# Kernel tuning notes

Hardware: AMD Instinct MI355X
Metric: run time of the kernel (lower is better)

The kernel has to match this reference:

```python
import jax, jax.numpy as jnp
import numpy as np

N, H, W, D = 4, 32, 32, 64
NH = 8
L = 4             # num_layers
DFF = 4 * D       # dim_feedforward
PRUNE_RATIO = 0.3
LN_EPS = 1e-5


def setup_inputs() -> dict:
    key = jax.random.key(0)
    ks = jax.random.split(key, 10)
    rn = lambda k, shape: (jax.random.normal(k, shape, dtype=jnp.float32) * 0.02)
    n_keep = int(D * PRUNE_RATIO)
    prune_mask = jnp.concatenate([jnp.ones((n_keep,), jnp.float32), jnp.zeros((D - n_keep,), jnp.float32)])
    return {
        "hsi_features": jax.random.normal(ks[0], (N, H, W, D), dtype=jnp.float32),
        "rgb_features": jax.random.normal(ks[1], (N, H, W, D), dtype=jnp.float32),
        "in_proj_w": rn(ks[2], (L, 3 * D, D)),
        "in_proj_b": jnp.zeros((L, 3 * D), jnp.float32),
        "out_w": rn(ks[3], (L, D, D)),
        "out_b": jnp.zeros((L, D), jnp.float32),
        "lin1_w": rn(ks[4], (L, DFF, D)),
        "lin1_b": jnp.zeros((L, DFF), jnp.float32),
        "lin2_w": rn(ks[5], (L, D, DFF)),
        "lin2_b": jnp.zeros((L, D), jnp.float32),
        "ln1_w": jnp.ones((L, D), jnp.float32),
        "ln1_b": jnp.zeros((L, D), jnp.float32),
        "ln2_w": jnp.ones((L, D), jnp.float32),
        "ln2_b": jnp.zeros((L, D), jnp.float32),
        "prune_mask": prune_mask,
    }


def _ln(x, w, b):
    mu = x.mean(-1, keepdims=True)
    var = ((x - mu) ** 2).mean(-1, keepdims=True)
    return (x - mu) * jax.lax.rsqrt(var + LN_EPS) * w + b


def _encoder_layer(x, p):
    # Post-LN TransformerEncoderLayer (torch default, eval mode -> no dropout).
    in_w, in_b, ow, ob, l1w, l1b, l2w, l2b, n1w, n1b, n2w, n2b = p
    M = x.shape[0]
    hd = D // NH
    qkv = x @ in_w.T + in_b                       # [M, 3D]
    q, k, v = jnp.split(qkv, 3, axis=-1)
    q = q.reshape(M, NH, hd).transpose(1, 0, 2)   # [NH, M, hd]
    k = k.reshape(M, NH, hd).transpose(1, 0, 2)
    v = v.reshape(M, NH, hd).transpose(1, 0, 2)
    scale = 1.0 / jnp.sqrt(jnp.float32(hd))
    att = jax.nn.softmax(jnp.einsum('hmd,hnd->hmn', q * scale, k), axis=-1)  # [NH, M, M]
    o = jnp.einsum('hmn,hnd->hmd', att, v).transpose(1, 0, 2).reshape(M, D)
    o = o @ ow.T + ob
    x = _ln(x + o, n1w, n1b)
    ff = jax.nn.relu(x @ l1w.T + l1b) @ l2w.T + l2b
    return _ln(x + ff, n2w, n2b)


def _mmd(x, y, sigma=1.0):
    # Gaussian-kernel MMD; ||a-b||^2 via norms + GEMM (no MxMxD intermediate).
    def gk_mean(a, b):
        d = (a * a).sum(-1)[:, None] + (b * b).sum(-1)[None, :] - 2.0 * (a @ b.T)
        return jnp.exp(-d / (2.0 * sigma ** 2)).mean()
    return gk_mean(x, x) + gk_mean(y, y) - 2.0 * gk_mean(x, y)


def _forward(hsi_features, rgb_features, in_proj_w, in_proj_b, out_w, out_b,
             lin1_w, lin1_b, lin2_w, lin2_b, ln1_w, ln1_b, ln2_w, ln2_b, prune_mask):
    Nb, Hh, Ww, C = hsi_features.shape
    x = hsi_features.reshape(-1, C)               # [M, D], M = N*H*W tokens (batch=1)
    for i in range(L):
        x = _encoder_layer(x, (in_proj_w[i], in_proj_b[i], out_w[i], out_b[i],
                               lin1_w[i], lin1_b[i], lin2_w[i], lin2_b[i],
                               ln1_w[i], ln1_b[i], ln2_w[i], ln2_b[i]))
    x = x * prune_mask
    mmd_loss = _mmd(x, rgb_features.reshape(-1, C))
    return x.reshape(Nb, Hh, Ww, C), mmd_loss


def reference(hsi_features, rgb_features, in_proj_w, in_proj_b, out_w, out_b,
              lin1_w, lin1_b, lin2_w, lin2_b, ln1_w, ln1_b, ln2_w, ln2_b, prune_mask):
    return _forward(hsi_features, rgb_features, in_proj_w, in_proj_b, out_w, out_b,
                    lin1_w, lin1_b, lin2_w, lin2_b, ln1_w, ln1_b, ln2_w, ln2_b, prune_mask)
```

## Files before the change

### kernel.cpp

```cpp
#include <hip/hip_runtime.h>

#define MT 4096
#define DM 64
#define NHEAD 8
#define HDIM 8
#define DFF 256
#define NLAYER 4
#define LN_EPS 1e-5f
#define ZSPLIT 8

#define QSCALE 0.51011784f
#define MMDC (-0.72134752f)

#if __has_builtin(__builtin_amdgcn_exp2f)
#define EXP2(x) __builtin_amdgcn_exp2f(x)
#else
#define EXP2(x) exp2f(x)
#endif

typedef __attribute__((ext_vector_type(8))) short bf16x8;
typedef __attribute__((ext_vector_type(4))) short bf16x4;
typedef __attribute__((ext_vector_type(4))) float f32x4;
typedef __attribute__((ext_vector_type(16))) float f32x16;
typedef __attribute__((ext_vector_type(4))) _Float16 f16x4;

__device__ __forceinline__ float wave_sum64(float v) {
#pragma unroll
  for (int m = 1; m < 64; m <<= 1) v += __shfl_xor(v, m, 64);
  return v;
}

__device__ __forceinline__ short f2bf(float x) {
  union { float f; unsigned u; } v; v.f = x;
  unsigned r = v.u + 0x7fffu + ((v.u >> 16) & 1u);
  return (short)(r >> 16);
}

__device__ __forceinline__ unsigned packbf2(float a, float b) {
  union { float f; unsigned u; } x, y; x.f = a; y.f = b;
  return __builtin_amdgcn_perm(y.u, x.u, 0x07060302u);
}

__global__ __launch_bounds__(256) void prep_kernel(
    const float* __restrict__ inw, float* __restrict__ Wti,
    const float* __restrict__ ow,  float* __restrict__ Wto,
    const float* __restrict__ l1w, float* __restrict__ Wt1,
    const float* __restrict__ l2w, float* __restrict__ Wt2,
    const float* __restrict__ rgb, short* __restrict__ rgbb, float* __restrict__ nrm,
    const float* __restrict__ hsi, const float* __restrict__ inb, float* __restrict__ x,
    _Float16* __restrict__ Qh, _Float16* __restrict__ Kh, short* __restrict__ Vtb) {
  const int bid = blockIdx.x;
  const int tid = threadIdx.x;
  if (bid >= 1216) {
    const int t0 = (bid - 1216) * 4;
    __shared__ float xr[4][DM];
    if (tid < 64) {
      float4 v = ((const float4*)(hsi + (size_t)t0 * DM))[tid];
      ((float4*)xr)[tid] = v;
      ((float4*)(x + (size_t)t0 * DM))[tid] = v;
    }
    __syncthreads();
    const int o = tid;
    if (o < 192) {
      float acc0 = inb[o], acc1 = acc0, acc2 = acc0, acc3 = acc0;
      const float* wrow = inw + (size_t)o * DM;
#pragma unroll 8
      for (int k4 = 0; k4 < 16; ++k4) {
        float4 w4 = *(const float4*)&wrow[k4 * 4];
        float4 a = *(const float4*)&xr[0][k4 * 4];
        acc0 += a.x * w4.x + a.y * w4.y + a.z * w4.z + a.w * w4.w;
        float4 b = *(const float4*)&xr[1][k4 * 4];
        acc1 += b.x * w4.x + b.y * w4.y + b.z * w4.z + b.w * w4.w;
        float4 c = *(const float4*)&xr[2][k4 * 4];
        acc2 += c.x * w4.x + c.y * w4.y + c.z * w4.z + c.w * w4.w;
        float4 d = *(const float4*)&xr[3][k4 * 4];
        acc3 += d.x * w4.x + d.y * w4.y + d.z * w4.z + d.w * w4.w;
      }
      if (o < 128) {
        const int c = o & 63, hh = c >> 3, ch = c & 7;
        _Float16* dst = (o < 64) ? Qh : Kh;
        const float sc = (o < 64) ? QSCALE : 1.0f;
        dst[((size_t)hh * MT + t0 + 0) * 8 + ch] = (_Float16)(acc0 * sc);
        dst[((size_t)hh * MT + t0 + 1) * 8 + ch] = (_Float16)(acc1 * sc);
        dst[((size_t)hh * MT + t0 + 2) * 8 + ch] = (_Float16)(acc2 * sc);
        dst[((size_t)hh * MT + t0 + 3) * 8 + ch] = (_Float16)(acc3 * sc);
      } else {
        const int c = o - 128;
        bf16x4 v = {f2bf(acc0), f2bf(acc1), f2bf(acc2), f2bf(acc3)};
        *(bf16x4*)&Vtb[(size_t)c * MT + t0] = v;
      }
    }
    return;
  }
  if (bid >= 192) {
    const int row = (bid - 192) * 4 + (tid >> 6);
    const int d = tid & 63;
    float v = rgb[(size_t)row * DM + d];
    rgbb[(size_t)row * DM + d] = f2bf(v);
    float s = wave_sum64(v * v);
    if (d == 0) nrm[MT + row] = s;
    return;
  }
  const float* src; float* dst; int R, C, r0, c0;
  if (bid < 48) {
    int l = bid / 12, t = bid % 12;
    src = inw + (size_t)l * 12288; dst = Wti + (size_t)l * 12288;
    R = 192; C = 64; c0 = (t % 2) * 32; r0 = (t / 2) * 32;
  } else if (bid < 64) {
    int idx = bid - 48, l = idx / 4, t = idx % 4;
    src = ow + (size_t)l * 4096; dst = Wto + (size_t)l * 4096;
    R = 64; C = 64; c0 = (t % 2) * 32; r0 = (t / 2) * 32;
  } else if (bid < 128) {
    int idx = bid - 64, l = idx / 16, t = idx % 16;
    src = l1w + (size_t)l * 16384; dst = Wt1 + (size_t)l * 16384;
    R = 256; C = 64; c0 = (t % 2) * 32; r0 = (t / 2) * 32;
  } else {
    int idx = bid - 128, l = idx / 16, t = idx % 16;
    src = l2w + (size_t)l * 16384; dst = Wt2 + (size_t)l * 16384;
    R = 64; C = 256; c0 = (t % 8) * 32; r0 = (t / 8) * 32;
  }
  __shared__ float tl[32][33];
  const int tx = tid & 31, ty = tid >> 5;
  for (int rr = ty; rr < 32; rr += 8)
    tl[rr][tx] = src[(size_t)(r0 + rr) * C + c0 + tx];
  __syncthreads();
  for (int idx = tid; idx < 1024; idx += 256) {
    const int k4l = idx >> 7, rem = idx & 127, ol = rem >> 2, j = rem & 3;
    dst[(((size_t)(c0 >> 2) + k4l) * R + r0 + ol) * 4 + j] = tl[ol][k4l * 4 + j];
  }
}

__global__ __launch_bounds__(256, 6) void attn_kernel(const _Float16* __restrict__ Qh,
                                                      const _Float16* __restrict__ Kh,
                                                      const short* __restrict__ Vtb,
                                                      float* __restrict__ pbuf,
                                                      float* __restrict__ lbuf) {
  const int h = blockIdx.y;
  const int qbase = blockIdx.x * 128;
  const int z = blockIdx.z;
  const int tid = threadIdx.x;
  const int wid = tid >> 6;
  const int lane = tid & 63;
  const int l31 = lane & 31;
  const int hi = lane >> 5;
  const int n = lane & 15;
  const int quad = lane >> 4;

  __shared__ short Klds[2][128 * 8];
  __shared__ short Vtlds[2][9 * 136];
  __shared__ short Plds[4][32 * 72];

  if (tid < 32) {
    bf16x8 ones = {0x3F80, 0x3F80, 0x3F80, 0x3F80, 0x3F80, 0x3F80, 0x3F80, 0x3F80};
    *(bf16x8*)&Vtlds[tid >> 4][8 * 136 + (tid & 15) * 8] = ones;
  }

  const f16x4 qb = *(const f16x4*)&Qh[((size_t)h * MT + qbase + wid * 32 + l31) * 8 + hi * 4];
  const bf16x8 zero8 = {0, 0, 0, 0, 0, 0, 0, 0};

  {
    const int k0 = z * 512;
    if (tid < 128) {
      *(bf16x8*)&Klds[0][tid * 8] = *(const bf16x8*)&Kh[((size_t)h * MT + k0 + tid) * 8];
    } else {
      const int t2 = tid - 128, ch = t2 >> 4, seg = t2 & 15;
      *(bf16x8*)&Vtlds[0][ch * 136 + seg * 8] =
          *(const bf16x8*)&Vtb[((size_t)h * 8 + ch) * MT + k0 + seg * 8];
    }
  }
  __syncthreads();

  f32x4 o_acc0 = {0.f, 0.f, 0.f, 0.f};
  f32x4 o_acc1 = {0.f, 0.f, 0.f, 0.f};

  for (int kt = 0; kt < 4; ++kt) {
    const int buf = kt & 1;
    if (kt < 3) {
      const int k1 = z * 512 + (kt + 1) * 128;
      if (tid < 128) {
        *(bf16x8*)&Klds[buf ^ 1][tid * 8] = *(const bf16x8*)&Kh[((size_t)h * MT + k1 + tid) * 8];
      } else {
        const int t2 = tid - 128, ch = t2 >> 4, seg = t2 & 15;
        *(bf16x8*)&Vtlds[buf ^ 1][ch * 136 + seg * 8] =
            *(const bf16x8*)&Vtb[((size_t)h * 8 + ch) * MT + k1 + seg * 8];
      }
    }

#pragma unroll
    for (int c32 = 0; c32 < 4; ++c32) {
      f16x4 ka = *(const f16x4*)&((const _Float16*)Klds[buf])[(c32 * 32 + l31) * 8 + hi * 4];
      f32x16 zf = {0.f, 0.f, 0.f, 0.f, 0.f, 0.f, 0.f, 0.f,
                   0.f, 0.f, 0.f, 0.f, 0.f, 0.f, 0.f, 0.f};
      f32x16 s = __builtin_amdgcn_mfma_f32_32x32x8f16(ka, qb, zf, 0, 0, 0);
      short* pw = &Plds[wid][l31 * 72 + c32 * 32 + 4 * hi];
#pragma unroll
      for (int rg = 0; rg < 4; ++rg) {
        unsigned lo = packbf2(EXP2(s[4 * rg + 0]), EXP2(s[4 * rg + 1]));
        unsigned hi2 = packbf2(EXP2(s[4 * rg + 2]), EXP2(s[4 * rg + 3]));
        uint2 pv = {lo, hi2};
        *(uint2*)(pw + rg * 8) = pv;
      }
      bf16x8 va = zero8;
      if (n < 9) va = *(const bf16x8*)&Vtlds[buf][n * 136 + c32 * 32 + quad * 8];
      bf16x8 p0 = *(const bf16x8*)&Plds[wid][n * 72 + c32 * 32 + quad * 8];
      o_acc0 = __builtin_amdgcn_mfma_f32_16x16x32_bf16(va, p0, o_acc0, 0, 0, 0);
      bf16x8 p1 = *(const bf16x8*)&Plds[wid][(n + 16) * 72 + c32 * 32 + quad * 8];
      o_acc1 = __builtin_amdgcn_mfma_f32_16x16x32_bf16(va, p1, o_acc1, 0, 0, 0);
    }
    __syncthreads();
  }

  const int tok0 = qbase + wid * 32 + n;
  if (quad < 2) {
    float4 v0 = {o_acc0[0], o_acc0[1], o_acc0[2], o_acc0[3]};
    *(float4*)&pbuf[((size_t)z * MT + tok0) * DM + h * 8 + quad * 4] = v0;
    float4 v1 = {o_acc1[0], o_acc1[1], o_acc1[2], o_acc1[3]};
    *(float4*)&pbuf[((size_t)z * MT + tok0 + 16) * DM + h * 8 + quad * 4] = v1;
  }
  if (quad == 2) {
    lbuf[(size_t)z * MT * 8 + (size_t)tok0 * 8 + h] = o_acc0[0];
    lbuf[(size_t)z * MT * 8 + (size_t)(tok0 + 16) * 8 + h] = o_acc1[0];
  }
}

__global__ __launch_bounds__(256) void dense_kernel(
    const float* __restrict__ pbuf, const float* __restrict__ lbuf,
    float* __restrict__ x,
    const float* __restrict__ Wto, const float* __restrict__ ob,
    const float* __restrict__ n1w, const float* __restrict__ n1b,
    const float* __restrict__ Wt1, const float* __restrict__ b1,
    const float* __restrict__ Wt2, const float* __restrict__ b2,
    const float* __restrict__ n2w, const float* __restrict__ n2b,
    const float* __restrict__ Wti, const float* __restrict__ inb,
    _Float16* __restrict__ Qh, _Float16* __restrict__ Kh, short* __restrict__ Vtb,
    int do_qkv,
    const float* __restrict__ mask, float* __restrict__ out,
    short* __restrict__ xmb, float* __restrict__ nrm, int do_final) {
  const int t0 = blockIdx.x * 8;
  const int tid = threadIdx.x;
  const int w = tid >> 6, d = tid & 63;

  __shared__ float orow[8][DM];
  __shared__ float x1[8][DM];
  __shared__ float fr[8][DFF];
  __shared__ float x2s[8][DM];

#pragma unroll
  for (int tt = 0; tt < 2; ++tt) {
    const int t = w + tt * 4, tok = t0 + t, h = d >> 3;
    float o = 0.f, l = 0.f;
#pragma unroll
    for (int z = 0; z < ZSPLIT; ++z) {
      o += pbuf[((size_t)z * MT + tok) * DM + d];
      l += lbuf[(size_t)z * MT * 8 + (size_t)tok * 8 + h];
    }
    orow[t][d] = o / l;
  }
  __syncthreads();

  {
    float acc[2] = {ob[d], ob[d]};
#pragma unroll 8
    for (int k4 = 0; k4 < 16; ++k4) {
      float4 w4 = ((const float4*)Wto)[k4 * 64 + d];
      float4 a = *(const float4*)&orow[w][k4 * 4];
      acc[0] += a.x * w4.x + a.y * w4.y + a.z * w4.z + a.w * w4.w;
      float4 b = *(const float4*)&orow[w + 4][k4 * 4];
      acc[1] += b.x * w4.x + b.y * w4.y + b.z * w4.z + b.w * w4.w;
    }
#pragma unroll
    for (int tt = 0; tt < 2; ++tt) {
      const int t = w + tt * 4, tok = t0 + t;
      float hv = x[(size_t)tok * DM + d] + acc[tt];
      float mu = wave_sum64(hv) * (1.0f / DM);
      float dv = hv - mu;
      float var = wave_sum64(dv * dv) * (1.0f / DM);
      x1[t][d] = dv * rsqrtf(var + LN_EPS) * n1w[d] + n1b[d];
    }
  }
  __syncthreads();

  {
    const int o = tid;
    float acc[8];
#pragma unroll
    for (int t = 0; t < 8; ++t) acc[t] = b1[o];
#pragma unroll 8
    for (int k4 = 0; k4 < 16; ++k4) {
      float4 w4 = ((const float4*)Wt1)[k4 * 256 + o];
#pragma unroll
      for (int t = 0; t < 8; ++t) {
        float4 a = *(const float4*)&x1[t][k4 * 4];
        acc[t] += a.x * w4.x + a.y * w4.y + a.z * w4.z + a.w * w4.w;
      }
    }
#pragma unroll
    for (int t = 0; t < 8; ++t) fr[t][o] = fmaxf(acc[t], 0.0f);
  }
  __syncthreads();

  {
    float acc[2] = {b2[d], b2[d]};
#pragma unroll 8
    for (int k4 = 0; k4 < 64; ++k4) {
      float4 w4 = ((const float4*)Wt2)[k4 * 64 + d];
      float4 a = *(const float4*)&fr[w][k4 * 4];
      acc[0] += a.x * w4.x + a.y * w4.y + a.z * w4.z + a.w * w4.w;
      float4 b = *(const float4*)&fr[w + 4][k4 * 4];
      acc[1] += b.x * w4.x + b.y * w4.y + b.z * w4.z + b.w * w4.w;
    }
#pragma unroll
    for (int tt = 0; tt < 2; ++tt) {
      const int t = w + tt * 4, tok = t0 + t;
      float hv = x1[t][d] + acc[tt];
      float mu = wave_sum64(hv) * (1.0f / DM);
      float dv = hv - mu;
      float var = wave_sum64(dv * dv) * (1.0f / DM);
      float v = dv * rsqrtf(var + LN_EPS) * n2w[d] + n2b[d];
      x2s[t][d] = v;
      x[(size_t)tok * DM + d] = v;
      if (do_final) {
        float pv = v * mask[d];
        out[(size_t)tok * DM + d] = pv;
        xmb[(size_t)tok * DM + d] = f2bf(pv);
        float s = wave_sum64(pv * pv);
        if (d == 0) nrm[tok] = s;
      }
    }
  }
  __syncthreads();

  if (do_qkv && tid < 192) {
    const int o = tid;
    float acc[8];
#pragma unroll
    for (int t = 0; t < 8; ++t) acc[t] = inb[o];
#pragma unroll 8
    for (int k4 = 0; k4 < 16; ++k4) {
      float4 w4 = ((const float4*)Wti)[k4 * 192 + o];
#pragma unroll
      for (int t = 0; t < 8; ++t) {
        float4 a = *(const float4*)&x2s[t][k4 * 4];
        acc[t] += a.x * w4.x + a.y * w4.y + a.z * w4.z + a.w * w4.w;
      }
    }
    if (o < 128) {
      const int c = o & 63, hh = c >> 3, ch = c & 7;
      _Float16* dst = (o < 64) ? Qh : Kh;
      const float sc = (o < 64) ? QSCALE : 1.0f;
#pragma unroll
      for (int t = 0; t < 8; ++t)
        dst[((size_t)hh * MT + t0 + t) * 8 + ch] = (_Float16)(acc[t] * sc);
    } else {
      bf16x8 v = {f2bf(acc[0]), f2bf(acc[1]), f2bf(acc[2]), f2bf(acc[3]),
                  f2bf(acc[4]), f2bf(acc[5]), f2bf(acc[6]), f2bf(acc[7])};
      *(bf16x8*)&Vtb[(size_t)(o - 128) * MT + t0] = v;
    }
  }
}

__global__ __launch_bounds__(256) void mmd_kernel(const short* __restrict__ xmb,
                                                  const short* __restrict__ rgbb,
                                                  const float* __restrict__ nrm,
                                                  float* __restrict__ partials) {
  const int bid = blockIdx.x;
  int p, bx, by;
  float coef;
  if (bid < 1024) {
    p = 2; bx = bid & 31; by = bid >> 5; coef = -2.0f;
  } else {
    const int t = bid - 1024;
    p = (t < 528) ? 0 : 1;
    const int u = (t < 528) ? t : t - 528;
    by = (int)((sqrtf(8.0f * (float)u + 1.0f) - 1.0f) * 0.5f);
    while ((by + 1) * (by + 2) / 2 <= u) ++by;
    while (by * (by + 1) / 2 > u) --by;
    bx = u - by * (by + 1) / 2;
    coef = (bx == by) ? 1.0f : 2.0f;
  }
  const short* A = (p == 1) ? rgbb : xmb;
  const short* B = (p == 0) ? xmb : rgbb;
  const float* nA = (p == 1) ? (nrm + MT) : nrm;
  const float* nB = (p == 0) ? nrm : (nrm + MT);
  const int i0 = bx * 128;
  const int j0 = by * 128;
  const int tid = threadIdx.x;
  const int wid = tid >> 6;
  const int lane = tid & 63;
  const int n = lane & 15;
  const int quad = lane >> 4;

  bf16x8 a0[2], a1[2];
  float na[2][4];
#pragma unroll
  for (int s = 0; s < 2; ++s) {
    const int arow = i0 + wid * 32 + s * 16 + n;
    a0[s] = *(const bf16x8*)&A[(size_t)arow * DM + quad * 8];
    a1[s] = *(const bf16x8*)&A[(size_t)arow * DM + 32 + quad * 8];
#pragma unroll
    for (int r = 0; r < 4; ++r) na[s][r] = nA[i0 + wid * 32 + s * 16 + quad * 4 + r];
  }
  bf16x8 b0[8], b1[8];
  float nb[8];
#pragma unroll
  for (int nt = 0; nt < 8; ++nt) {
    const int brow = j0 + nt * 16 + n;
    b0[nt] = *(const bf16x8*)&B[(size_t)brow * DM + quad * 8];
    b1[nt] = *(const bf16x8*)&B[(size_t)brow * DM + 32 + quad * 8];
    nb[nt] = nB[j0 + nt * 16 + n];
  }

  float local = 0.f;
#pragma unroll
  for (int nt = 0; nt < 8; ++nt) {
#pragma unroll
    for (int s = 0; s < 2; ++s) {
      f32x4 zf = {0.f, 0.f, 0.f, 0.f};
      f32x4 d4 = __builtin_amdgcn_mfma_f32_16x16x32_bf16(a0[s], b0[nt], zf, 0, 0, 0);
      d4 = __builtin_amdgcn_mfma_f32_16x16x32_bf16(a1[s], b1[nt], d4, 0, 0, 0);
#pragma unroll
      for (int r = 0; r < 4; ++r) {
        float dist = na[s][r] + nb[nt] - 2.0f * d4[r];
        local += EXP2(MMDC * dist);
      }
    }
  }

  float tot = wave_sum64(local);
  __shared__ float wpart[4];
  if (lane == 0) wpart[wid] = tot;
  __syncthreads();
  if (tid == 0)
    partials[bid] = coef * (wpart[0] + wpart[1] + wpart[2] + wpart[3]);
}

__global__ __launch_bounds__(256) void reducefin_kernel(const float* __restrict__ partials,
                                                        float* __restrict__ out) {
  const int tid = threadIdx.x;
  float s = 0.f;
  for (int i = tid; i < 2080; i += 256) s += partials[i];
  s = wave_sum64(s);
  __shared__ float L[4];
  if ((tid & 63) == 0) L[tid >> 6] = s;
  __syncthreads();
  if (tid == 0) {
    const float invn = 1.0f / ((float)MT * (float)MT);
    out[(size_t)MT * DM] = (L[0] + L[1] + L[2] + L[3]) * invn;
  }
}

extern "C" void kernel_launch(void* const* d_in, const int* in_sizes, int n_in,
                              void* d_out, int out_size, void* d_ws, size_t ws_size,
                              hipStream_t stream) {
  const float* hsi  = (const float*)d_in[0];
  const float* rgb  = (const float*)d_in[1];
  const float* inw  = (const float*)d_in[2];
  const float* inb  = (const float*)d_in[3];
  const float* ow   = (const float*)d_in[4];
  const float* obv  = (const float*)d_in[5];
  const float* l1w  = (const float*)d_in[6];
  const float* l1b  = (const float*)d_in[7];
  const float* l2w  = (const float*)d_in[8];
  const float* l2b  = (const float*)d_in[9];
  const float* n1w  = (const float*)d_in[10];
  const float* n1b  = (const float*)d_in[11];
  const float* n2w  = (const float*)d_in[12];
  const float* n2b  = (const float*)d_in[13];
  const float* mask = (const float*)d_in[14];
  float* out = (float*)d_out;

  float* ws      = (float*)d_ws;
  float* x       = ws;
  float* pbuf    = ws + 262144;
  float* lbuf    = ws + 2359296;
  float* nrm     = ws + 2621440;
  float* parts   = ws + 2629632;
  float* Wti     = ws + 2633728;
  float* Wto     = ws + 2682880;
  float* Wt1     = ws + 2699264;
  float* Wt2     = ws + 2764800;
  short* xmb     = (short*)(ws + 2830336);
  short* rgbb    = (short*)(ws + 2961408);
  _Float16* Qh   = (_Float16*)(ws + 3092480);
  _Float16* Kh   = (_Float16*)(ws + 3223552);
  short* Vtb     = (short*)(ws + 3354624);

  prep_kernel<<<192 + MT / 4 + MT / 4, 256, 0, stream>>>(
      inw, Wti, ow, Wto, l1w, Wt1, l2w, Wt2, rgb, rgbb, nrm,
      hsi, inb, x, Qh, Kh, Vtb);

  for (int i = 0; i < NLAYER; ++i) {
    attn_kernel<<<dim3(MT / 128, NHEAD, ZSPLIT), 256, 0, stream>>>(Qh, Kh, Vtb, pbuf, lbuf);
    const int last = (i == NLAYER - 1);
    dense_kernel<<<MT / 8, 256, 0, stream>>>(
        pbuf, lbuf, x,
        Wto + (size_t)i * DM * DM, obv + (size_t)i * DM,
        n1w + (size_t)i * DM, n1b + (size_t)i * DM,
        Wt1 + (size_t)i * DFF * DM, l1b + (size_t)i * DFF,
        Wt2 + (size_t)i * DM * DFF, l2b + (size_t)i * DM,
        n2w + (size_t)i * DM, n2b + (size_t)i * DM,
        Wti + (size_t)(last ? 0 : (i + 1)) * 192 * DM,
        inb + (size_t)(last ? 0 : (i + 1)) * 192,
        Qh, Kh, Vtb, !last,
        mask, out, xmb, nrm, last);
  }

  mmd_kernel<<<2080, 256, 0, stream>>>(xmb, rgbb, nrm, parts);
  reducefin_kernel<<<1, 256, 0, stream>>>(parts, out);
}
```

Baseline: 311.9 us.

## Halve attention key split and give dense kernel one wave per token

```diff
diff --git a/kernel.cpp b/kernel.cpp
--- a/kernel.cpp
+++ b/kernel.cpp
@@ -7,7 +7,7 @@
 #define DFF 256
 #define NLAYER 4
 #define LN_EPS 1e-5f
-#define ZSPLIT 8
+#define ZSPLIT 4
 
 #define QSCALE 0.51011784f
 #define MMDC (-0.72134752f)
@@ -159,7 +159,7 @@
   const bf16x8 zero8 = {0, 0, 0, 0, 0, 0, 0, 0};
 
   {
-    const int k0 = z * 512;
+    const int k0 = z * 1024;
     if (tid < 128) {
       *(bf16x8*)&Klds[0][tid * 8] = *(const bf16x8*)&Kh[((size_t)h * MT + k0 + tid) * 8];
     } else {
@@ -173,10 +173,10 @@
   f32x4 o_acc0 = {0.f, 0.f, 0.f, 0.f};
   f32x4 o_acc1 = {0.f, 0.f, 0.f, 0.f};
 
-  for (int kt = 0; kt < 4; ++kt) {
+  for (int kt = 0; kt < 8; ++kt) {
     const int buf = kt & 1;
-    if (kt < 3) {
-      const int k1 = z * 512 + (kt + 1) * 128;
+    if (kt < 7) {
+      const int k1 = z * 1024 + (kt + 1) * 128;
       if (tid < 128) {
         *(bf16x8*)&Klds[buf ^ 1][tid * 8] = *(const bf16x8*)&Kh[((size_t)h * MT + k1 + tid) * 8];
       } else {
@@ -223,7 +223,7 @@
   }
 }
 
-__global__ __launch_bounds__(256) void dense_kernel(
+__global__ __launch_bounds__(512) void dense_kernel(
     const float* __restrict__ pbuf, const float* __restrict__ lbuf,
     float* __restrict__ x,
     const float* __restrict__ Wto, const float* __restrict__ ob,
@@ -245,116 +245,106 @@
   __shared__ float fr[8][DFF];
   __shared__ float x2s[8][DM];
 
-#pragma unroll
-  for (int tt = 0; tt < 2; ++tt) {
-    const int t = w + tt * 4, tok = t0 + t, h = d >> 3;
+  {
+    const int tok = t0 + w, h = d >> 3;
     float o = 0.f, l = 0.f;
 #pragma unroll
     for (int z = 0; z < ZSPLIT; ++z) {
       o += pbuf[((size_t)z * MT + tok) * DM + d];
       l += lbuf[(size_t)z * MT * 8 + (size_t)tok * 8 + h];
     }
-    orow[t][d] = o / l;
+    orow[w][d] = o / l;
   }
   __syncthreads();
 
   {
-    float acc[2] = {ob[d], ob[d]};
+    const int tok = t0 + w;
+    float acc = ob[d];
 #pragma unroll 8
     for (int k4 = 0; k4 < 16; ++k4) {
       float4 w4 = ((const float4*)Wto)[k4 * 64 + d];
       float4 a = *(const float4*)&orow[w][k4 * 4];
-      acc[0] += a.x * w4.x + a.y * w4.y + a.z * w4.z + a.w * w4.w;
-      float4 b = *(const float4*)&orow[w + 4][k4 * 4];
-      acc[1] += b.x * w4.x + b.y * w4.y + b.z * w4.z + b.w * w4.w;
-    }
-#pragma unroll
-    for (int tt = 0; tt < 2; ++tt) {
-      const int t = w + tt * 4, tok = t0 + t;
-      float hv = x[(size_t)tok * DM + d] + acc[tt];
-      float mu = wave_sum64(hv) * (1.0f / DM);
-      float dv = hv - mu;
-      float var = wave_sum64(dv * dv) * (1.0f / DM);
-      x1[t][d] = dv * rsqrtf(var + LN_EPS) * n1w[d] + n1b[d];
-    }
+      acc += a.x * w4.x + a.y * w4.y + a.z * w4.z + a.w * w4.w;
+    }
+    float hv = x[(size_t)tok * DM + d] + acc;
+    float mu = wave_sum64(hv) * (1.0f / DM);
+    float dv = hv - mu;
+    float var = wave_sum64(dv * dv) * (1.0f / DM);
+    x1[w][d] = dv * rsqrtf(var + LN_EPS) * n1w[d] + n1b[d];
   }
   __syncthreads();
 
   {
-    const int o = tid;
-    float acc[8];
-#pragma unroll
-    for (int t = 0; t < 8; ++t) acc[t] = b1[o];
+    const int g = tid >> 8, o = tid & 255;
+    float acc[4];
+#pragma unroll
+    for (int t = 0; t < 4; ++t) acc[t] = b1[o];
 #pragma unroll 8
     for (int k4 = 0; k4 < 16; ++k4) {
       float4 w4 = ((const float4*)Wt1)[k4 * 256 + o];
 #pragma unroll
-      for (int t = 0; t < 8; ++t) {
-        float4 a = *(const float4*)&x1[t][k4 * 4];
+      for (int t = 0; t < 4; ++t) {
+        float4 a = *(const float4*)&x1[g * 4 + t][k4 * 4];
         acc[t] += a.x * w4.x + a.y * w4.y + a.z * w4.z + a.w * w4.w;
       }
     }
 #pragma unroll
-    for (int t = 0; t < 8; ++t) fr[t][o] = fmaxf(acc[t], 0.0f);
+    for (int t = 0; t < 4; ++t) fr[g * 4 + t][o] = fmaxf(acc[t], 0.0f);
   }
   __syncthreads();
 
   {
-    float acc[2] = {b2[d], b2[d]};
+    const int tok = t0 + w;
+    float acc = b2[d];
 #pragma unroll 8
     for (int k4 = 0; k4 < 64; ++k4) {
       float4 w4 = ((const float4*)Wt2)[k4 * 64 + d];
       float4 a = *(const float4*)&fr[w][k4 * 4];
-      acc[0] += a.x * w4.x + a.y * w4.y + a.z * w4.z + a.w * w4.w;
-      float4 b = *(const float4*)&fr[w + 4][k4 * 4];
-      acc[1] += b.x * w4.x + b.y * w4.y + b.z * w4.z + b.w * w4.w;
-    }
-#pragma unroll
-    for (int tt = 0; tt < 2; ++tt) {
-      const int t = w + tt * 4, tok = t0 + t;
-      float hv = x1[t][d] + acc[tt];
-      float mu = wave_sum64(hv) * (1.0f / DM);
-      float dv = hv - mu;
-      float var = wave_sum64(dv * dv) * (1.0f / DM);
-      float v = dv * rsqrtf(var + LN_EPS) * n2w[d] + n2b[d];
-      x2s[t][d] = v;
-      x[(size_t)tok * DM + d] = v;
-      if (do_final) {
-        float pv = v * mask[d];
-        out[(size_t)tok * DM + d] = pv;
-        xmb[(size_t)tok * DM + d] = f2bf(pv);
-        float s = wave_sum64(pv * pv);
-        if (d == 0) nrm[tok] = s;
-      }
-    }
-  }
-  __syncthreads();
-
-  if (do_qkv && tid < 192) {
-    const int o = tid;
-    float acc[8];
-#pragma unroll
-    for (int t = 0; t < 8; ++t) acc[t] = inb[o];
+      acc += a.x * w4.x + a.y * w4.y + a.z * w4.z + a.w * w4.w;
+    }
+    float hv = x1[w][d] + acc;
+    float mu = wave_sum64(hv) * (1.0f / DM);
+    float dv = hv - mu;
+    float var = wave_sum64(dv * dv) * (1.0f / DM);
+    float v = dv * rsqrtf(var + LN_EPS) * n2w[d] + n2b[d];
+    x2s[w][d] = v;
+    x[(size_t)tok * DM + d] = v;
+    if (do_final) {
+      float pv = v * mask[d];
+      out[(size_t)tok * DM + d] = pv;
+      xmb[(size_t)tok * DM + d] = f2bf(pv);
+      float s = wave_sum64(pv * pv);
+      if (d == 0) nrm[tok] = s;
+    }
+  }
+  __syncthreads();
+
+  if (do_qkv) {
+    const int g = tid >> 8, o = tid & 255;
+    if (o < 192) {
+      float acc[4];
+#pragma unroll
+      for (int t = 0; t < 4; ++t) acc[t] = inb[o];
 #pragma unroll 8
-    for (int k4 = 0; k4 < 16; ++k4) {
-      float4 w4 = ((const float4*)Wti)[k4 * 192 + o];
-#pragma unroll
-      for (int t = 0; t < 8; ++t) {
-        float4 a = *(const float4*)&x2s[t][k4 * 4];
-        acc[t] += a.x * w4.x + a.y * w4.y + a.z * w4.z + a.w * w4.w;
-      }
-    }
-    if (o < 128) {
-      const int c = o & 63, hh = c >> 3, ch = c & 7;
-      _Float16* dst = (o < 64) ? Qh : Kh;
-      const float sc = (o < 64) ? QSCALE : 1.0f;
-#pragma unroll
-      for (int t = 0; t < 8; ++t)
-        dst[((size_t)hh * MT + t0 + t) * 8 + ch] = (_Float16)(acc[t] * sc);
-    } else {
-      bf16x8 v = {f2bf(acc[0]), f2bf(acc[1]), f2bf(acc[2]), f2bf(acc[3]),
-                  f2bf(acc[4]), f2bf(acc[5]), f2bf(acc[6]), f2bf(acc[7])};
-      *(bf16x8*)&Vtb[(size_t)(o - 128) * MT + t0] = v;
+      for (int k4 = 0; k4 < 16; ++k4) {
+        float4 w4 = ((const float4*)Wti)[k4 * 192 + o];
+#pragma unroll
+        for (int t = 0; t < 4; ++t) {
+          float4 a = *(const float4*)&x2s[g * 4 + t][k4 * 4];
+          acc[t] += a.x * w4.x + a.y * w4.y + a.z * w4.z + a.w * w4.w;
+        }
+      }
+      if (o < 128) {
+        const int c = o & 63, hh = c >> 3, ch = c & 7;
+        _Float16* dst = (o < 64) ? Qh : Kh;
+        const float sc = (o < 64) ? QSCALE : 1.0f;
+#pragma unroll
+        for (int t = 0; t < 4; ++t)
+          dst[((size_t)hh * MT + t0 + g * 4 + t) * 8 + ch] = (_Float16)(acc[t] * sc);
+      } else {
+        bf16x4 v = {f2bf(acc[0]), f2bf(acc[1]), f2bf(acc[2]), f2bf(acc[3])};
+        *(bf16x4*)&Vtb[(size_t)(o - 128) * MT + t0 + g * 4] = v;
+      }
     }
   }
 }
@@ -472,18 +462,18 @@
   float* ws      = (float*)d_ws;
   float* x       = ws;
   float* pbuf    = ws + 262144;
-  float* lbuf    = ws + 2359296;
-  float* nrm     = ws + 2621440;
-  float* parts   = ws + 2629632;
-  float* Wti     = ws + 2633728;
-  float* Wto     = ws + 2682880;
-  float* Wt1     = ws + 2699264;
-  float* Wt2     = ws + 2764800;
-  short* xmb     = (short*)(ws + 2830336);
-  short* rgbb    = (short*)(ws + 2961408);
-  _Float16* Qh   = (_Float16*)(ws + 3092480);
-  _Float16* Kh   = (_Float16*)(ws + 3223552);
-  short* Vtb     = (short*)(ws + 3354624);
+  float* lbuf    = ws + 1310720;
+  float* nrm     = ws + 1441792;
+  float* parts   = ws + 1449984;
+  float* Wti     = ws + 1454080;
+  float* Wto     = ws + 1503232;
+  float* Wt1     = ws + 1519616;
+  float* Wt2     = ws + 1585152;
+  short* xmb     = (short*)(ws + 1650688);
+  short* rgbb    = (short*)(ws + 1781760);
+  _Float16* Qh   = (_Float16*)(ws + 1912832);
+  _Float16* Kh   = (_Float16*)(ws + 2043904);
+  short* Vtb     = (short*)(ws + 2174976);
 
   prep_kernel<<<192 + MT / 4 + MT / 4, 256, 0, stream>>>(
       inw, Wti, ow, Wto, l1w, Wt1, l2w, Wt2, rgb, rgbb, nrm,
@@ -492,7 +482,7 @@
   for (int i = 0; i < NLAYER; ++i) {
     attn_kernel<<<dim3(MT / 128, NHEAD, ZSPLIT), 256, 0, stream>>>(Qh, Kh, Vtb, pbuf, lbuf);
     const int last = (i == NLAYER - 1);
-    dense_kernel<<<MT / 8, 256, 0, stream>>>(
+    dense_kernel<<<MT / 8, 512, 0, stream>>>(
         pbuf, lbuf, x,
         Wto + (size_t)i * DM * DM, obv + (size_t)i * DM,
         n1w + (size_t)i * DM, n1b + (size_t)i * DM,
```

After: 291.3 us. 1.07x faster.
